# Kernel tuning notes

Measured on AMD Instinct MI355X. Metric: run time of the kernel, lower is better.

Reference implementation:

```python
import jax, jax.numpy as jnp
from jax import lax
import numpy as np


def setup_inputs() -> dict:
    key = jax.random.key(0)
    x = jax.random.normal(key, (16, 1, 1536, 1536), dtype=jnp.float32)
    weight = jnp.ones((1, 1, 3, 3), dtype=jnp.float32) / 9.0
    return {"x": x, "weight": weight}


def _box3x3(z, weight):
    # z: (N, 1, H, W); zero padding=1 (torch conv2d default pad mode)
    return lax.conv_general_dilated(
        z, weight, window_strides=(1, 1), padding=((1, 1), (1, 1)),
        dimension_numbers=("NCHW", "OIHW", "NCHW"))


def _eig2x2(Axx, Axy, Ayy):
    # closed-form eigendecomposition of [[Axx, Axy], [Axy, Ayy]]
    T = Axx + Ayy
    D = Axx * Ayy - Axy * Axy
    s = jnp.sqrt(jnp.abs(T * T * 0.25 - D))
    l1 = T * 0.5 + s
    l2 = T * 0.5 - s
    e11 = l1 - Ayy
    e12 = Axy
    e21 = l2 - Ayy
    e22 = Axy
    small = jnp.abs(Axy) < 1e-9
    e11 = jnp.where(small, 1.0, e11)
    e12 = jnpp_zero = jnp.where(small, 0.0, e12)
    e21 = jnp.where(small, 0.0, e21)
    e22 = jnp.where(small, 1.0, e22)
    # sort so that the eigenvalue with smaller magnitude comes first
    lt = jnp.abs(l1) < jnp.abs(l2)
    lambda1 = jnp.where(lt, l1, l2)
    lambda2 = jnp.where(lt, l2, l1)
    e11_ = jnp.where(lt, e11, e21)
    e12_ = jnp.where(lt, e12, e22)
    e21_ = jnp.where(lt, e21, e11)
    e22_ = jnp.where(lt, e22, e12)
    # NOTE: original torch code has a typo (`labmda2_`), so only lambda1 gets ReLU
    lambda1 = jax.nn.relu(lambda1)
    return lambda1, lambda2, e11_, e12_, e21_, e22_


def reference(x, weight):
    n, c, h, w = x.shape
    # gx[..., 0] = x[..., 1] - x[..., 0]; gx[..., j] = x[..., j-1] - x[..., j]
    gx = jnp.concatenate([x[:, :, :, 1:2], x[:, :, :, :-1]], axis=3) - x
    gy = jnp.concatenate([x[:, :, 1:2, :], x[:, :, :-1, :]], axis=2) - x
    # per-channel box filter then mean over channels (c == 1 here)
    def smooth(z):
        zf = z.reshape(n * c, 1, h, w)
        out = _box3x3(zf, weight).reshape(n, c, h, w)
        return jnp.mean(out, axis=1)  # (N, H, W)
    Axx = smooth(gx * gx)
    Axy = smooth(gx * gy)
    Ayy = smooth(gy * gy)
    return _eig2x2(Axx, Axy, Ayy)
```

## Files before the change

### kernel.cpp

```cpp
#include <hip/hip_runtime.h>


typedef float f32x4 __attribute__((ext_vector_type(4)));
typedef float f32x2 __attribute__((ext_vector_type(2)));

constexpr int N_ = 16, H = 1536, W = 1536;

__device__ __forceinline__ void eig_row(
    const float S_xx[6], const float S_xy[6], const float S_yy[6],
    float* __restrict__ op, size_t PLANE) {
    f32x4 o_l1, o_l2, o_e11, o_e12, o_e21, o_e22;
    const float inv9 = 1.0f / 9.0f;
#pragma unroll
    for (int k = 0; k < 4; ++k) {
        const float Axx = (S_xx[k] + S_xx[k + 1] + S_xx[k + 2]) * inv9;
        const float Axy = (S_xy[k] + S_xy[k + 1] + S_xy[k + 2]) * inv9;
        const float Ayy = (S_yy[k] + S_yy[k + 1] + S_yy[k + 2]) * inv9;

        const float T  = Axx + Ayy;
        const float Dd = Axx * Ayy - Axy * Axy;
        const float s  = __builtin_amdgcn_sqrtf(fabsf(T * T * 0.25f - Dd));
        const float l1 = T * 0.5f + s;
        const float l2 = T * 0.5f - s;

        float e11 = l1 - Ayy, e12 = Axy;
        float e21 = l2 - Ayy, e22 = Axy;
        const bool small = fabsf(Axy) < 1e-9f;
        e11 = small ? 1.0f : e11;
        e12 = small ? 0.0f : e12;
        e21 = small ? 0.0f : e21;
        e22 = small ? 1.0f : e22;

        const bool lt = fabsf(l1) < fabsf(l2);
        o_l1[k]  = fmaxf(lt ? l1 : l2, 0.0f);
        o_l2[k]  = lt ? l2 : l1;
        o_e11[k] = lt ? e11 : e21;
        o_e12[k] = lt ? e12 : e22;
        o_e21[k] = lt ? e21 : e11;
        o_e22[k] = lt ? e22 : e12;
    }
    __builtin_nontemporal_store(o_l1,  reinterpret_cast<f32x4*>(op));
    __builtin_nontemporal_store(o_l2,  reinterpret_cast<f32x4*>(op + PLANE));
    __builtin_nontemporal_store(o_e11, reinterpret_cast<f32x4*>(op + 2 * PLANE));
    __builtin_nontemporal_store(o_e12, reinterpret_cast<f32x4*>(op + 3 * PLANE));
    __builtin_nontemporal_store(o_e21, reinterpret_cast<f32x4*>(op + 4 * PLANE));
    __builtin_nontemporal_store(o_e22, reinterpret_cast<f32x4*>(op + 5 * PLANE));
}

__global__ __launch_bounds__(256, 4)
void lsa_kernel(const float* __restrict__ x, float* __restrict__ out) {
    const int tid  = threadIdx.x;
    const int rsub = tid >> 6;
    const int csub = tid & 63;
    const int P0   = blockIdx.y * 8 + 2 * rsub;
    const int q0   = blockIdx.x * 256 + 4 * csub;
    const int n    = blockIdx.z;

    const size_t HW = (size_t)H * W;
    const size_t PLANE = (size_t)N_ * HW;
    const float* __restrict__ xn = x + (size_t)n * HW;

    float S0xx[6], S0xy[6], S0yy[6];
    float S1xx[6], S1xy[6], S1yy[6];

    const bool interior = (P0 >= 2) & (P0 <= H - 3) & (q0 >= 2) & (q0 <= W - 6);

    if (interior) {
        float xv[5][8];
        const float* rp = xn + (size_t)(P0 - 2) * W + (q0 - 2);
#pragma unroll
        for (int d = 0; d < 5; ++d) {
            const f32x2 a = *reinterpret_cast<const f32x2*>(rp);
            const f32x4 b = *reinterpret_cast<const f32x4*>(rp + 2);
            const f32x2 c = *reinterpret_cast<const f32x2*>(rp + 6);
            xv[d][0] = a.x; xv[d][1] = a.y;
            xv[d][2] = b.x; xv[d][3] = b.y; xv[d][4] = b.z; xv[d][5] = b.w;
            xv[d][6] = c.x; xv[d][7] = c.y;
            rp += W;
        }
#pragma unroll
        for (int m = 0; m < 6; ++m) {
            S0xx[m] = 0.f; S0xy[m] = 0.f; S0yy[m] = 0.f;
            S1xx[m] = 0.f; S1xy[m] = 0.f; S1yy[m] = 0.f;
        }
#pragma unroll
        for (int t = 0; t < 4; ++t) {
#pragma unroll
            for (int m = 0; m < 6; ++m) {
                const float xc = xv[t + 1][m + 1];
                const float xl = xv[t + 1][m];
                const float xu = xv[t][m + 1];
                const float gx = xl - xc;
                const float gy = xu - xc;
                const float pxx = gx * gx;
                const float pxy = gx * gy;
                const float pyy = gy * gy;
                if (t < 3) { S0xx[m] += pxx; S0xy[m] += pxy; S0yy[m] += pyy; }
                if (t > 0) { S1xx[m] += pxx; S1xy[m] += pxy; S1yy[m] += pyy; }
            }
        }
    } else {
#pragma unroll
        for (int r = 0; r < 2; ++r) {
            float* Sxx = r ? S1xx : S0xx;
            float* Sxy = r ? S1xy : S0xy;
            float* Syy = r ? S1yy : S0yy;
            const int pr = P0 + r;
#pragma unroll
            for (int m = 0; m < 6; ++m) {
                const int q = q0 - 1 + m;
                float sxx = 0.f, sxy = 0.f, syy = 0.f;
                if (q >= 0 && q < W) {
#pragma unroll
                    for (int d = 0; d < 3; ++d) {
                        const int p = pr - 1 + d;
                        if (p >= 0 && p < H) {
                            const float* prow = xn + (size_t)p * W;
                            const float xc = prow[q];
                            const float xl = (q == 0) ? prow[1] : prow[q - 1];
                            const float xu = (p == 0) ? xn[(size_t)W + q] : prow[q - W];
                            const float gx = xl - xc;
                            const float gy = xu - xc;
                            sxx = fmaf(gx, gx, sxx);
                            sxy = fmaf(gx, gy, sxy);
                            syy = fmaf(gy, gy, syy);
                        }
                    }
                }
                Sxx[m] = sxx; Sxy[m] = sxy; Syy[m] = syy;
            }
        }
    }

    float* op = out + (size_t)n * HW + (size_t)P0 * W + q0;
    eig_row(S0xx, S0xy, S0yy, op, PLANE);
    eig_row(S1xx, S1xy, S1yy, op + W, PLANE);
}

extern "C" void kernel_launch(void* const* d_in, const int* in_sizes, int n_in,
                              void* d_out, int out_size, void* d_ws, size_t ws_size,
                              hipStream_t stream) {
    const float* x = (const float*)d_in[0];
    float* out = (float*)d_out;

    dim3 grid(W / 256, H / 8, N_);
    dim3 block(256);
    lsa_kernel<<<grid, block, 0, stream>>>(x, out);
}
```

Baseline: 171.7 us.

## Compute four output rows per thread with rolling row buffer and streamed stores

Each thread now produces four output rows instead of two, so the 2-row halo is shared over more outputs and fewer rows of input are loaded per output. A two-row rolling register buffer is used, the next row's load is issued while the current one is processed, and each finished row's eigen results are stored right away. The grid halves in the y dimension. This cuts redundant global loads, in exchange for fewer blocks and possibly more register pressure.

```diff
diff --git a/kernel.cpp b/kernel.cpp
--- a/kernel.cpp
+++ b/kernel.cpp
@@ -5,6 +5,15 @@
 typedef float f32x2 __attribute__((ext_vector_type(2)));
 
 constexpr int N_ = 16, H = 1536, W = 1536;
+
+__device__ __forceinline__ void load_row8(const float* __restrict__ p, float d[8]) {
+    const f32x2 a = *reinterpret_cast<const f32x2*>(p);
+    const f32x4 b = *reinterpret_cast<const f32x4*>(p + 2);
+    const f32x2 c = *reinterpret_cast<const f32x2*>(p + 6);
+    d[0] = a.x; d[1] = a.y;
+    d[2] = b.x; d[3] = b.y; d[4] = b.z; d[5] = b.w;
+    d[6] = c.x; d[7] = c.y;
+}
 
 __device__ __forceinline__ void eig_row(
     const float S_xx[6], const float S_xy[6], const float S_yy[6],
@@ -50,61 +59,66 @@
 __global__ __launch_bounds__(256, 4)
 void lsa_kernel(const float* __restrict__ x, float* __restrict__ out) {
     const int tid  = threadIdx.x;
-    const int rsub = tid >> 6;
-    const int csub = tid & 63;
-    const int P0   = blockIdx.y * 8 + 2 * rsub;
-    const int q0   = blockIdx.x * 256 + 4 * csub;
+    const int wv   = tid >> 6;
+    const int lane = tid & 63;
+    const int P0   = blockIdx.y * 16 + 4 * wv;
+    const int q0   = blockIdx.x * 256 + 4 * lane;
     const int n    = blockIdx.z;
 
     const size_t HW = (size_t)H * W;
     const size_t PLANE = (size_t)N_ * HW;
     const float* __restrict__ xn = x + (size_t)n * HW;
+    float* const ob = out + (size_t)n * HW + (size_t)P0 * W + q0;
 
-    float S0xx[6], S0xy[6], S0yy[6];
-    float S1xx[6], S1xy[6], S1yy[6];
-
-    const bool interior = (P0 >= 2) & (P0 <= H - 3) & (q0 >= 2) & (q0 <= W - 6);
+    const bool interior = (P0 >= 2) & (P0 <= H - 5) & (q0 >= 2) & (q0 <= W - 6);
 
     if (interior) {
-        float xv[5][8];
+        float Sxx[4][6], Sxy[4][6], Syy[4][6];
+        float xrow[2][8];
         const float* rp = xn + (size_t)(P0 - 2) * W + (q0 - 2);
+        load_row8(rp, xrow[0]);
+        load_row8(rp + W, xrow[1]);
+
 #pragma unroll
-        for (int d = 0; d < 5; ++d) {
-            const f32x2 a = *reinterpret_cast<const f32x2*>(rp);
-            const f32x4 b = *reinterpret_cast<const f32x4*>(rp + 2);
-            const f32x2 c = *reinterpret_cast<const f32x2*>(rp + 6);
-            xv[d][0] = a.x; xv[d][1] = a.y;
-            xv[d][2] = b.x; xv[d][3] = b.y; xv[d][4] = b.z; xv[d][5] = b.w;
-            xv[d][6] = c.x; xv[d][7] = c.y;
-            rp += W;
-        }
-#pragma unroll
-        for (int m = 0; m < 6; ++m) {
-            S0xx[m] = 0.f; S0xy[m] = 0.f; S0yy[m] = 0.f;
-            S1xx[m] = 0.f; S1xy[m] = 0.f; S1yy[m] = 0.f;
-        }
-#pragma unroll
-        for (int t = 0; t < 4; ++t) {
+        for (int t = 0; t < 6; ++t) {
+            const float* xu_row = xrow[t & 1];
+            const float* xc_row = xrow[(t + 1) & 1];
+            float pxx[6], pxy[6], pyy[6];
 #pragma unroll
             for (int m = 0; m < 6; ++m) {
-                const float xc = xv[t + 1][m + 1];
-                const float xl = xv[t + 1][m];
-                const float xu = xv[t][m + 1];
+                const float xc = xc_row[m + 1];
+                const float xl = xc_row[m];
+                const float xu = xu_row[m + 1];
                 const float gx = xl - xc;
                 const float gy = xu - xc;
-                const float pxx = gx * gx;
-                const float pxy = gx * gy;
-                const float pyy = gy * gy;
-                if (t < 3) { S0xx[m] += pxx; S0xy[m] += pxy; S0yy[m] += pyy; }
-                if (t > 0) { S1xx[m] += pxx; S1xy[m] += pxy; S1yy[m] += pyy; }
+                pxx[m] = gx * gx; pxy[m] = gx * gy; pyy[m] = gy * gy;
+            }
+            if (t < 5) load_row8(rp + (size_t)(t + 2) * W, xrow[t & 1]);
+#pragma unroll
+            for (int r = 0; r < 4; ++r) {
+                if (t >= r && t <= r + 2) {
+                    if (t == r) {
+#pragma unroll
+                        for (int m = 0; m < 6; ++m) {
+                            Sxx[r][m] = pxx[m]; Sxy[r][m] = pxy[m]; Syy[r][m] = pyy[m];
+                        }
+                    } else {
+#pragma unroll
+                        for (int m = 0; m < 6; ++m) {
+                            Sxx[r][m] += pxx[m]; Sxy[r][m] += pxy[m]; Syy[r][m] += pyy[m];
+                        }
+                    }
+                }
+            }
+            if (t >= 2) {
+                const int r = t - 2;
+                eig_row(Sxx[r], Sxy[r], Syy[r], ob + (size_t)r * W, PLANE);
             }
         }
     } else {
 #pragma unroll
-        for (int r = 0; r < 2; ++r) {
-            float* Sxx = r ? S1xx : S0xx;
-            float* Sxy = r ? S1xy : S0xy;
-            float* Syy = r ? S1yy : S0yy;
+        for (int r = 0; r < 4; ++r) {
+            float Sxx[6], Sxy[6], Syy[6];
             const int pr = P0 + r;
 #pragma unroll
             for (int m = 0; m < 6; ++m) {
@@ -129,12 +143,9 @@
                 }
                 Sxx[m] = sxx; Sxy[m] = sxy; Syy[m] = syy;
             }
+            eig_row(Sxx, Sxy, Syy, ob + (size_t)r * W, PLANE);
         }
     }
-
-    float* op = out + (size_t)n * HW + (size_t)P0 * W + q0;
-    eig_row(S0xx, S0xy, S0yy, op, PLANE);
-    eig_row(S1xx, S1xy, S1yy, op + W, PLANE);
 }
 
 extern "C" void kernel_launch(void* const* d_in, const int* in_sizes, int n_in,
@@ -143,7 +154,7 @@
     const float* x = (const float*)d_in[0];
     float* out = (float*)d_out;
 
-    dim3 grid(W / 256, H / 8, N_);
+    dim3 grid(W / 256, H / 16, N_);
     dim3 block(256);
     lsa_kernel<<<grid, block, 0, stream>>>(x, out);
 }
```

Result: slower. 227.3 us (+32.4%).
